# Kernel optimization log

Measured on AMD Instinct MI355X. Metric: run time of the kernel, lower is better.

The kernel has to match this reference:

```python
import jax, jax.numpy as jnp
import numpy as np
from jax import lax

D_MODEL, D_INNER, D_CONV, DT_RANK, D_STATE, SEQ_LEN = 1024, 2048, 4, 64, 16, 4096


def setup_inputs() -> dict:
    key = jax.random.key(0)
    ks = jax.random.split(key, 9)
    s = 0.02
    x = jax.random.normal(ks[0], (SEQ_LEN, D_MODEL), dtype=jnp.float32)
    W_in = jax.random.normal(ks[1], (2 * D_INNER, D_MODEL), dtype=jnp.float32) * s
    conv_w = jax.random.normal(ks[2], (D_INNER, 1, D_CONV), dtype=jnp.float32) * 0.2  # depthwise (O,I/g,K)
    conv_b = jax.random.normal(ks[3], (D_INNER,), dtype=jnp.float32) * s
    W_x = jax.random.normal(ks[4], (DT_RANK + 2 * D_STATE, D_INNER), dtype=jnp.float32) * s
    W_dt = jax.random.normal(ks[5], (D_INNER, DT_RANK), dtype=jnp.float32) * s
    b_dt = jax.random.normal(ks[6], (D_INNER,), dtype=jnp.float32) * s
    # canonical S4D-real init: A[d, n] = n+1 -> A_log = log(1..d_state), tiled over d_inner
    A_log = jnp.log(jnp.tile(jnp.arange(1, D_STATE + 1, dtype=jnp.float32), (D_INNER, 1)))
    D = jnp.ones((D_INNER,), dtype=jnp.float32)
    W_out = jax.random.normal(ks[7], (D_MODEL, D_INNER), dtype=jnp.float32) * s
    return {"x": x, "W_in": W_in, "conv_w": conv_w, "conv_b": conv_b,
            "W_x": W_x, "W_dt": W_dt, "b_dt": b_dt, "A_log": A_log, "D": D,
            "W_out": W_out}


def _causal_depthwise_conv(x_ld, conv_w, conv_b):
    # x_ld: (L, d_inner). eqx Conv1d with padding=d_conv-1 then [:, :L] == left-pad causal conv.
    k = conv_w.shape[-1]
    xp = jnp.pad(x_ld, ((k - 1, 0), (0, 0)))  # (L+k-1, d)
    lhs = xp.T[None]  # (1, d, L+k-1)
    out = lax.conv_general_dilated(
        lhs, conv_w, window_strides=(1,), padding='VALID',
        dimension_numbers=('NCH', 'OIH', 'NCH'),
        feature_group_count=x_ld.shape[1])  # (1, d, L)
    return (out[0] + conv_b[:, None]).T  # (L, d)


def reference(x, W_in, conv_w, conv_b, W_x, W_dt, b_dt, A_log, D, W_out):
    L = x.shape[0]
    d_inner, d_state = A_log.shape
    dt_rank = W_dt.shape[1]

    xr = x @ W_in.T                      # (L, 2*d_inner)
    xi, res = jnp.split(xr, 2, axis=-1)  # each (L, d_inner)
    xs = jax.nn.silu(_causal_depthwise_conv(xi, conv_w, conv_b))  # (L, d_inner)

    # selective SSM
    dbl = xs @ W_x.T                     # (L, dt_rank + 2*d_state)
    dt_in, B, C = jnp.split(dbl, [dt_rank, dt_rank + d_state], axis=-1)
    delta = jax.nn.softplus(dt_in @ W_dt.T + b_dt)       # (L, d_inner)
    A = -jnp.exp(A_log)                                  # (d_inner, d_state)
    dA = jnp.exp(delta[:, :, None] * A[None])            # (L, d, n)
    dBu = delta[:, :, None] * B[:, None, :] * xs[:, :, None]  # (L, d, n)

    def step(h, ab):
        a, b = ab
        h = a * h + b
        return h, h

    _, hs = lax.scan(step, jnp.zeros((d_inner, d_state), dtype=x.dtype), (dA, dBu))
    y = jnp.einsum('ldn,ln->ld', hs, C) + xs * D         # (L, d_inner)

    y = y * jax.nn.silu(res)
    return y @ W_out.T                                   # (L, d_model)
```

## Files before the change

kernel.cpp:

```cpp
#include <hip/hip_runtime.h>
#include <cstdint>
#include <cstddef>

#define LSEQ 4096
#define DM 1024
#define DI 2048
#define DCONV 4
#define DRNK 64
#define DSTATE 16
#define DXW 96
#define NCH 64
#define CLEN 64
#define KSPLIT 8

typedef unsigned short ushort_t;
typedef __bf16 bfx8 __attribute__((ext_vector_type(8)));
typedef float  fx4  __attribute__((ext_vector_type(4)));
typedef ushort_t usx8 __attribute__((ext_vector_type(8)));

__device__ __forceinline__ float siluf(float x) { return x / (1.f + __expf(-x)); }
__device__ __forceinline__ float softplusf(float x) {
  return fmaxf(x, 0.f) + log1pf(__expf(-fabsf(x)));
}
__device__ __forceinline__ ushort_t f2b(float x) {
  __bf16 b = (__bf16)x;
  return __builtin_bit_cast(ushort_t, b);
}
__device__ __forceinline__ float b2f(ushort_t u) {
  unsigned int x = ((unsigned int)u) << 16;
  return __builtin_bit_cast(float, x);
}
__device__ __forceinline__ void async16(const void* g, void* l) {
  __builtin_amdgcn_global_load_lds(
      (const __attribute__((address_space(1))) unsigned int*)g,
      (__attribute__((address_space(3))) unsigned int*)l, 16, 0, 0);
}

template <int EPI, int BN>
__global__ __launch_bounds__(256) void gemm_bf16(
    const ushort_t* __restrict__ A, int lda,
    const ushort_t* __restrict__ B, int ldb,
    void* __restrict__ Cv, int ldc, int K,
    const float* __restrict__ bias)
{
  constexpr int NJ = BN / 32;
  __shared__ ushort_t As[128 * 32];
  __shared__ ushort_t Bs[BN * 32];
  const int tid  = threadIdx.x;
  const int m0   = blockIdx.y * 128, n0 = blockIdx.x * BN;
  const int lane = tid & 63;
  const int wave = tid >> 6;
  const int wm   = (wave >> 1) * 64, wn = (wave & 1) * (BN / 2);
  const int lm   = lane & 15;
  const int r0 = tid >> 2;
  const int cswz = (((tid & 3) ^ ((r0 >> 1) & 3))) * 8;
  const int swz = (((lane >> 4) ^ ((lm >> 1) & 3))) * 8;

  fx4 acc[4][NJ] = {};

  const ushort_t* ga = A + (size_t)(m0 + r0) * lda + cswz;
  const ushort_t* gb = B + (size_t)(n0 + r0) * ldb + cswz;
  ushort_t* la0 = &As[r0 * 32 + (tid & 3) * 8];
  ushort_t* la1 = &As[(r0 + 64) * 32 + (tid & 3) * 8];
  ushort_t* lb0 = &Bs[r0 * 32 + (tid & 3) * 8];
  ushort_t* lb1 = (BN == 128) ? &Bs[(r0 + 64) * 32 + (tid & 3) * 8] : nullptr;

  for (int k0 = 0; k0 < K; k0 += 32) {
    async16(ga + k0, la0);
    async16(ga + (size_t)64 * lda + k0, la1);
    async16(gb + k0, lb0);
    if (BN == 128) async16(gb + (size_t)64 * ldb + k0, lb1);
    __syncthreads();

    bfx8 af[4], bfr[NJ];
#pragma unroll
    for (int i = 0; i < 4; ++i)
      af[i] = *(const bfx8*)&As[(wm + i * 16 + lm) * 32 + swz];
#pragma unroll
    for (int j = 0; j < NJ; ++j)
      bfr[j] = *(const bfx8*)&Bs[(wn + j * 16 + lm) * 32 + swz];
#pragma unroll
    for (int i = 0; i < 4; ++i)
#pragma unroll
      for (int j = 0; j < NJ; ++j)
        acc[i][j] = __builtin_amdgcn_mfma_f32_16x16x32_bf16(af[i], bfr[j], acc[i][j], 0, 0, 0);
    __syncthreads();
  }

  const int crow = (lane >> 4) * 4;
  const int ccol = lane & 15;
#pragma unroll
  for (int i = 0; i < 4; ++i)
#pragma unroll
    for (int r = 0; r < 4; ++r) {
      const size_t rowoff = (size_t)(m0 + wm + i * 16 + crow + r) * ldc + n0 + wn + ccol;
      if (EPI == 1) {
        ushort_t* cp = (ushort_t*)Cv + rowoff;
#pragma unroll
        for (int j = 0; j < NJ; ++j) cp[j * 16] = f2b(acc[i][j][r]);
      } else if (EPI == 2) {
        ushort_t* cp = (ushort_t*)Cv + rowoff;
        const int nb = n0 + wn + ccol;
#pragma unroll
        for (int j = 0; j < NJ; ++j)
          cp[j * 16] = f2b(softplusf(acc[i][j][r] + bias[nb + j * 16]));
      } else {
        float* cp = (float*)Cv + rowoff;
#pragma unroll
        for (int j = 0; j < NJ; ++j) cp[j * 16] = acc[i][j][r];
      }
    }
}

__global__ __launch_bounds__(256) void gemm_dbl(
    const ushort_t* __restrict__ A, const ushort_t* __restrict__ B,
    float* __restrict__ P)
{
  __shared__ ushort_t As[128 * 32];
  __shared__ ushort_t Bs[128 * 32];
  const int tid  = threadIdx.x;
  const int m0   = blockIdx.y * 128;
  const int lane = tid & 63;
  const int wave = tid >> 6;
  const int wm   = (wave >> 1) * 64, wn = (wave & 1) * 48;
  const int lm   = lane & 15;
  const int r0 = tid >> 2;
  const int cswz = (((tid & 3) ^ ((r0 >> 1) & 3))) * 8;
  const int swz  = (((lane >> 4) ^ ((lm >> 1) & 3))) * 8;
  const int kbeg = blockIdx.z * (DI / KSPLIT);

  fx4 acc[4][3] = {};

  const int brow1 = (r0 + 64 < DXW) ? r0 + 64 : DXW - 1;
  const ushort_t* ga  = A + (size_t)(m0 + r0) * DI + kbeg + cswz;
  const ushort_t* gb0 = B + (size_t)r0 * DI + kbeg + cswz;
  const ushort_t* gb1 = B + (size_t)brow1 * DI + kbeg + cswz;
  ushort_t* la0 = &As[r0 * 32 + (tid & 3) * 8];
  ushort_t* la1 = &As[(r0 + 64) * 32 + (tid & 3) * 8];
  ushort_t* lb0 = &Bs[r0 * 32 + (tid & 3) * 8];
  ushort_t* lb1 = &Bs[(r0 + 64) * 32 + (tid & 3) * 8];

  for (int k0 = 0; k0 < DI / KSPLIT; k0 += 32) {
    async16(ga + k0, la0);
    async16(ga + (size_t)64 * DI + k0, la1);
    async16(gb0 + k0, lb0);
    async16(gb1 + k0, lb1);
    __syncthreads();

    bfx8 af[4], bfr[3];
#pragma unroll
    for (int i = 0; i < 4; ++i)
      af[i] = *(const bfx8*)&As[(wm + i * 16 + lm) * 32 + swz];
#pragma unroll
    for (int j = 0; j < 3; ++j)
      bfr[j] = *(const bfx8*)&Bs[(wn + j * 16 + lm) * 32 + swz];
#pragma unroll
    for (int i = 0; i < 4; ++i)
#pragma unroll
      for (int j = 0; j < 3; ++j)
        acc[i][j] = __builtin_amdgcn_mfma_f32_16x16x32_bf16(af[i], bfr[j], acc[i][j], 0, 0, 0);
    __syncthreads();
  }

  float* base = P + (size_t)blockIdx.z * LSEQ * DXW;
  const int crow = (lane >> 4) * 4;
  const int ccol = lane & 15;
#pragma unroll
  for (int i = 0; i < 4; ++i)
#pragma unroll
    for (int r = 0; r < 4; ++r) {
      float* cp = base + (size_t)(m0 + wm + i * 16 + crow + r) * DXW + wn + ccol;
#pragma unroll
      for (int j = 0; j < 3; ++j)
        cp[j * 16] = acc[i][j][r];
    }
}

__global__ __launch_bounds__(256) void reduce_dbl(
    const float* __restrict__ P, ushort_t* __restrict__ dtb,
    float* __restrict__ dblBC)
{
  const int f = blockIdx.x * 256 + threadIdx.x;
  float s = 0.f;
#pragma unroll
  for (int z = 0; z < KSPLIT; ++z) s += P[(size_t)z * LSEQ * DXW + f];
  const int l = f / DXW;
  const int c = f - l * DXW;
  if (c < DRNK) dtb[(size_t)l * DRNK + c] = f2b(s);
  else          dblBC[(size_t)l * 32 + (c - DRNK)] = s;
}

#define CSZ0 (LSEQ * DM)
#define CSZ1 (2 * DI * DM)
#define CSZ2 (DM * DI)
#define CSZ3 (DXW * DI)
#define CSZ4 (DI * DRNK)
#define CTOT (CSZ0 + CSZ1 + CSZ2 + CSZ3 + CSZ4)

__global__ __launch_bounds__(256) void cast_all(
    const float* __restrict__ x, const float* __restrict__ W_in,
    const float* __restrict__ W_out, const float* __restrict__ W_x,
    const float* __restrict__ W_dt,
    ushort_t* __restrict__ xb, ushort_t* __restrict__ W_inb,
    ushort_t* __restrict__ W_outb, ushort_t* __restrict__ W_xb,
    ushort_t* __restrict__ W_dtb)
{
  int i = (blockIdx.x * 256 + threadIdx.x) * 4;
  if (i >= CTOT) return;
  const float* src; ushort_t* dst;
  if (i < CSZ0) { src = x + i; dst = xb + i; }
  else if (i < CSZ0 + CSZ1) { int o = i - CSZ0; src = W_in + o; dst = W_inb + o; }
  else if (i < CSZ0 + CSZ1 + CSZ2) { int o = i - CSZ0 - CSZ1; src = W_out + o; dst = W_outb + o; }
  else if (i < CSZ0 + CSZ1 + CSZ2 + CSZ3) { int o = i - CSZ0 - CSZ1 - CSZ2; src = W_x + o; dst = W_xb + o; }
  else { int o = i - CSZ0 - CSZ1 - CSZ2 - CSZ3; src = W_dt + o; dst = W_dtb + o; }
  float4 v = *(const float4*)src;
  ushort4 o4;
  o4.x = f2b(v.x); o4.y = f2b(v.y); o4.z = f2b(v.z); o4.w = f2b(v.w);
  *(ushort4*)dst = o4;
}

__global__ __launch_bounds__(256) void conv2(
    const ushort_t* __restrict__ xrb, const float* __restrict__ cw,
    const float* __restrict__ cb, ushort_t* __restrict__ xsb)
{
  const int d0 = threadIdx.x * 8;
  const int l0 = blockIdx.x * 8;

  float4 w[8];
#pragma unroll
  for (int j = 0; j < 8; ++j) w[j] = *(const float4*)(cw + (size_t)(d0 + j) * DCONV);
  float cbv[8];
  *(float4*)&cbv[0] = *(const float4*)(cb + d0);
  *(float4*)&cbv[4] = *(const float4*)(cb + d0 + 4);

  float h0[8], h1[8], h2[8];
#pragma unroll
  for (int j = 0; j < 8; ++j) { h0[j] = 0.f; h1[j] = 0.f; h2[j] = 0.f; }
  if (l0 >= 3) {
    usx8 u0 = *(const usx8*)(xrb + (size_t)(l0 - 3) * (2 * DI) + d0);
    usx8 u1 = *(const usx8*)(xrb + (size_t)(l0 - 2) * (2 * DI) + d0);
    usx8 u2 = *(const usx8*)(xrb + (size_t)(l0 - 1) * (2 * DI) + d0);
#pragma unroll
    for (int j = 0; j < 8; ++j) { h0[j] = b2f(u0[j]); h1[j] = b2f(u1[j]); h2[j] = b2f(u2[j]); }
  }

#pragma unroll
  for (int i = 0; i < 8; ++i) {
    const int l = l0 + i;
    usx8 uc = *(const usx8*)(xrb + (size_t)l * (2 * DI) + d0);
    float c[8];
#pragma unroll
    for (int j = 0; j < 8; ++j) c[j] = b2f(uc[j]);
    usx8 o;
#pragma unroll
    for (int j = 0; j < 8; ++j) {
      float acc = cbv[j];
      acc = fmaf(w[j].x, h0[j], acc);
      acc = fmaf(w[j].y, h1[j], acc);
      acc = fmaf(w[j].z, h2[j], acc);
      acc = fmaf(w[j].w, c[j], acc);
      o[j] = f2b(siluf(acc));
    }
    *(usx8*)(xsb + (size_t)l * DI + d0) = o;
#pragma unroll
    for (int j = 0; j < 8; ++j) { h0[j] = h1[j]; h1[j] = h2[j]; h2[j] = c[j]; }
  }
}

__device__ __forceinline__ bool chain_ok(const float* Av) {
  bool ok = true;
#pragma unroll
  for (int n = 0; n < DSTATE; ++n)
    ok = ok && (fabsf(Av[n] + (float)(n + 1)) < 1e-4f);
  return ok;
}

__global__ __launch_bounds__(256) void scan_pass1(
    const ushort_t* __restrict__ deltab, const ushort_t* __restrict__ xsb,
    const float* __restrict__ dblBC, const float* __restrict__ A_log,
    float* __restrict__ cP, float* __restrict__ cS)
{
  const int tid = threadIdx.x;
  const int g = blockIdx.x;
  const int c = blockIdx.y;
  const int d = g * 256 + tid;
  __shared__ ushort_t Dsh[CLEN * 256];
  __shared__ ushort_t Ush[CLEN * 256];
  __shared__ float Bsh[CLEN][DSTATE];

  const size_t rowbase = (size_t)(c * CLEN) * DI + g * 256;
  for (int i = tid; i < CLEN * 32; i += 256) {
    const int l = i >> 5;
    const int o = (i & 31) * 8;
    *(usx8*)&Dsh[l * 256 + o] = *(const usx8*)(deltab + rowbase + (size_t)l * DI + o);
    *(usx8*)&Ush[l * 256 + o] = *(const usx8*)(xsb   + rowbase + (size_t)l * DI + o);
  }
  for (int i = tid; i < CLEN * DSTATE; i += 256) {
    const int l = i >> 4, n = i & 15;
    Bsh[l][n] = dblBC[(size_t)(c * CLEN + l) * 32 + n];
  }
  __syncthreads();

  float Av[DSTATE], h[DSTATE];
#pragma unroll
  for (int n = 0; n < DSTATE; ++n) {
    Av[n] = -__expf(A_log[d * DSTATE + n]);
    h[n] = 0.f;
  }
  const size_t base = (size_t)c * DI * DSTATE + (size_t)d * DSTATE;

  if (chain_ok(Av)) {
    float sd = 0.f;
    for (int l = 0; l < CLEN; ++l) {
      const float dlt = b2f(Dsh[l * 256 + tid]);
      const float du = dlt * b2f(Ush[l * 256 + tid]);
      sd += dlt;
      const float q = __expf(-dlt);
      float dAn = 1.f;
#pragma unroll
      for (int n = 0; n < DSTATE; ++n) {
        dAn *= q;
        h[n] = fmaf(dAn, h[n], du * Bsh[l][n]);
      }
    }
    const float Qc = __expf(-sd);
    float Pn = 1.f;
#pragma unroll
    for (int n = 0; n < DSTATE; ++n) {
      Pn *= Qc;
      cP[base + n] = Pn; cS[base + n] = h[n];
    }
  } else {
    float P[DSTATE];
#pragma unroll
    for (int n = 0; n < DSTATE; ++n) P[n] = 1.f;
    for (int l = 0; l < CLEN; ++l) {
      const float dlt = b2f(Dsh[l * 256 + tid]);
      const float du = dlt * b2f(Ush[l * 256 + tid]);
#pragma unroll
      for (int n = 0; n < DSTATE; ++n) {
        const float dA = __expf(dlt * Av[n]);
        h[n] = fmaf(dA, h[n], du * Bsh[l][n]);
        P[n] *= dA;
      }
    }
#pragma unroll
    for (int n = 0; n < DSTATE; ++n) { cP[base + n] = P[n]; cS[base + n] = h[n]; }
  }
}

__global__ __launch_bounds__(256) void scan_pass2(
    const float* __restrict__ cP, const float* __restrict__ cS,
    float* __restrict__ ch0)
{
  const int dn = blockIdx.x * 256 + threadIdx.x;
  float h = 0.f;
  for (int c = 0; c < NCH; ++c) {
    const size_t o = (size_t)c * DI * DSTATE + dn;
    const float p = cP[o], s = cS[o];
    ch0[o] = h;
    h = fmaf(p, h, s);
  }
}

__global__ __launch_bounds__(256) void scan_pass3(
    const ushort_t* __restrict__ deltab, const ushort_t* __restrict__ xsb,
    const float* __restrict__ dblBC, const float* __restrict__ A_log,
    const float* __restrict__ ch0, const float* __restrict__ Dp,
    const ushort_t* __restrict__ xrb, ushort_t* __restrict__ y1b)
{
  const int tid = threadIdx.x;
  const int g = blockIdx.x;
  const int c = blockIdx.y;
  const int d = g * 256 + tid;
  __shared__ ushort_t Dsh[CLEN * 256];
  __shared__ ushort_t Ush[CLEN * 256];
  __shared__ float Bsh[CLEN][DSTATE];
  __shared__ float Csh[CLEN][DSTATE];

  const size_t rowbase = (size_t)(c * CLEN) * DI + g * 256;
  for (int i = tid; i < CLEN * 32; i += 256) {
    const int l = i >> 5;
    const int o = (i & 31) * 8;
    *(usx8*)&Dsh[l * 256 + o] = *(const usx8*)(deltab + rowbase + (size_t)l * DI + o);
    *(usx8*)&Ush[l * 256 + o] = *(const usx8*)(xsb   + rowbase + (size_t)l * DI + o);
  }
  for (int i = tid; i < CLEN * DSTATE; i += 256) {
    const int l = i >> 4, n = i & 15;
    const size_t row = (size_t)(c * CLEN + l) * 32;
    Bsh[l][n] = dblBC[row + n];
    Csh[l][n] = dblBC[row + 16 + n];
  }
  __syncthreads();

  float Av[DSTATE], h[DSTATE];
  const size_t base = (size_t)c * DI * DSTATE + (size_t)d * DSTATE;
#pragma unroll
  for (int n = 0; n < DSTATE; ++n) {
    Av[n] = -__expf(A_log[d * DSTATE + n]);
    h[n] = ch0[base + n];
  }
  const float Dd = Dp[d];
  const ushort_t* resp = xrb + (size_t)(c * CLEN) * (2 * DI) + DI + d;
  ushort_t* yp = y1b + (size_t)(c * CLEN) * DI + d;

  if (chain_ok(Av)) {
    for (int l = 0; l < CLEN; ++l) {
      const float dlt = b2f(Dsh[l * 256 + tid]);
      const float u = b2f(Ush[l * 256 + tid]);
      const float du = dlt * u;
      const float q = __expf(-dlt);
      float dAn = 1.f;
      float y = 0.f;
#pragma unroll
      for (int n = 0; n < DSTATE; ++n) {
        dAn *= q;
        h[n] = fmaf(dAn, h[n], du * Bsh[l][n]);
        y = fmaf(h[n], Csh[l][n], y);
      }
      y = fmaf(u, Dd, y);
      const float res = b2f(resp[(size_t)l * (2 * DI)]);
      yp[(size_t)l * DI] = f2b(y * siluf(res));
    }
  } else {
    for (int l = 0; l < CLEN; ++l) {
      const float dlt = b2f(Dsh[l * 256 + tid]);
      const float u = b2f(Ush[l * 256 + tid]);
      const float du = dlt * u;
      float y = 0.f;
#pragma unroll
      for (int n = 0; n < DSTATE; ++n) {
        const float dA = __expf(dlt * Av[n]);
        h[n] = fmaf(dA, h[n], du * Bsh[l][n]);
        y = fmaf(h[n], Csh[l][n], y);
      }
      y = fmaf(u, Dd, y);
      const float res = b2f(resp[(size_t)l * (2 * DI)]);
      yp[(size_t)l * DI] = f2b(y * siluf(res));
    }
  }
}

extern "C" void kernel_launch(void* const* d_in, const int* in_sizes, int n_in,
                              void* d_out, int out_size, void* d_ws, size_t ws_size,
                              hipStream_t stream) {
  (void)in_sizes; (void)n_in; (void)out_size; (void)ws_size;
  const float* x      = (const float*)d_in[0];
  const float* W_in   = (const float*)d_in[1];
  const float* conv_w = (const float*)d_in[2];
  const float* conv_b = (const float*)d_in[3];
  const float* W_x    = (const float*)d_in[4];
  const float* W_dt   = (const float*)d_in[5];
  const float* b_dt   = (const float*)d_in[6];
  const float* A_log  = (const float*)d_in[7];
  const float* Dp     = (const float*)d_in[8];
  const float* W_out  = (const float*)d_in[9];
  float* out = (float*)d_out;

  float* ws    = (float*)d_ws;
  float* cP    = ws;
  float* cS    = cP + (size_t)NCH * DI * DSTATE;
  ushort_t* deltab = (ushort_t*)(cS + (size_t)NCH * DI * DSTATE);
  ushort_t* xrb   = deltab + (size_t)LSEQ * DI;
  ushort_t* xsb   = xrb   + (size_t)LSEQ * 2 * DI;
  ushort_t* y1b   = xsb   + (size_t)LSEQ * DI;
  ushort_t* xb    = y1b   + (size_t)LSEQ * DI;
  ushort_t* W_inb = xb    + (size_t)LSEQ * DM;
  ushort_t* W_outb= W_inb + (size_t)2 * DI * DM;
  ushort_t* W_xb  = W_outb+ (size_t)DM * DI;
  ushort_t* W_dtb = W_xb  + (size_t)DXW * DI;
  ushort_t* dtb   = W_dtb + (size_t)DI * DRNK;
  float* dblBC = (float*)(dtb + (size_t)LSEQ * DRNK);
  float* partial = cP;
  float* ch0 = cP;

  hipLaunchKernelGGL(cast_all, dim3((CTOT / 4 + 255) / 256), dim3(256), 0, stream,
                     x, W_in, W_out, W_x, W_dt, xb, W_inb, W_outb, W_xb, W_dtb);

  hipLaunchKernelGGL(HIP_KERNEL_NAME(gemm_bf16<1, 128>),
                     dim3((2 * DI) / 128, LSEQ / 128), dim3(256), 0, stream,
                     xb, DM, W_inb, DM, (void*)xrb, 2 * DI, DM, nullptr);

  hipLaunchKernelGGL(conv2, dim3(LSEQ / 8), dim3(256), 0, stream,
                     xrb, conv_w, conv_b, xsb);

  hipLaunchKernelGGL(gemm_dbl, dim3(1, LSEQ / 128, KSPLIT), dim3(256), 0, stream,
                     xsb, W_xb, partial);
  hipLaunchKernelGGL(reduce_dbl, dim3((LSEQ * DXW) / 256), dim3(256), 0, stream,
                     partial, dtb, dblBC);

  hipLaunchKernelGGL(HIP_KERNEL_NAME(gemm_bf16<2, 128>),
                     dim3(DI / 128, LSEQ / 128), dim3(256), 0, stream,
                     dtb, DRNK, W_dtb, DRNK, (void*)deltab, DI, DRNK, b_dt);

  hipLaunchKernelGGL(scan_pass1, dim3(DI / 256, NCH), dim3(256), 0, stream,
                     deltab, xsb, dblBC, A_log, cP, cS);
  hipLaunchKernelGGL(scan_pass2, dim3((DI * DSTATE) / 256), dim3(256), 0, stream,
                     cP, cS, ch0);
  hipLaunchKernelGGL(scan_pass3, dim3(DI / 256, NCH), dim3(256), 0, stream,
                     deltab, xsb, dblBC, A_log, ch0, Dp, xrb, y1b);

  hipLaunchKernelGGL(HIP_KERNEL_NAME(gemm_bf16<0, 64>),
                     dim3(DM / 64, LSEQ / 128), dim3(256), 0, stream,
                     y1b, DI, W_outb, DI, (void*)out, DM, DI, nullptr);
}
```

Before: 309.0 us.

## Fuse three-pass chunked scan into one kernel with inter-block atomic flags

Merges the per-chunk scan, the cross-chunk prefix pass and the output scan into a single kernel. Blocks publish chunk summaries and signal through per-group atomic counters; a subset of blocks runs the cross-chunk prefix and signals completion while the others wait. The delta and xs tiles are loaded into shared memory once instead of twice, and two kernel launches are removed. In exchange it relies on all 512 blocks being resident at the same time for the spin-waits to make progress, adds busy-waiting, and bounds the spin loops with a timeout that could silently let blocks proceed with incomplete data.

```diff
diff --git a/kernel.cpp b/kernel.cpp
--- a/kernel.cpp
+++ b/kernel.cpp
@@ -203,8 +203,9 @@
     const float* __restrict__ W_dt,
     ushort_t* __restrict__ xb, ushort_t* __restrict__ W_inb,
     ushort_t* __restrict__ W_outb, ushort_t* __restrict__ W_xb,
-    ushort_t* __restrict__ W_dtb)
+    ushort_t* __restrict__ W_dtb, int* __restrict__ flags)
 {
+  if (blockIdx.x == 0 && threadIdx.x < 16) flags[threadIdx.x] = 0;
   int i = (blockIdx.x * 256 + threadIdx.x) * 4;
   if (i >= CTOT) return;
   const float* src; ushort_t* dst;
@@ -275,100 +276,16 @@
   return ok;
 }
 
-__global__ __launch_bounds__(256) void scan_pass1(
+__global__ __launch_bounds__(256) void scan_fused(
     const ushort_t* __restrict__ deltab, const ushort_t* __restrict__ xsb,
     const float* __restrict__ dblBC, const float* __restrict__ A_log,
-    float* __restrict__ cP, float* __restrict__ cS)
+    const float* __restrict__ Dp, const ushort_t* __restrict__ xrb,
+    ushort_t* __restrict__ y1b,
+    float* __restrict__ cP, float* __restrict__ cS, float* __restrict__ ch0,
+    int* __restrict__ flags)
 {
-  const int tid = threadIdx.x;
-  const int g = blockIdx.x;
-  const int c = blockIdx.y;
-  const int d = g * 256 + tid;
-  __shared__ ushort_t Dsh[CLEN * 256];
-  __shared__ ushort_t Ush[CLEN * 256];
-  __shared__ float Bsh[CLEN][DSTATE];
-
-  const size_t rowbase = (size_t)(c * CLEN) * DI + g * 256;
-  for (int i = tid; i < CLEN * 32; i += 256) {
-    const int l = i >> 5;
-    const int o = (i & 31) * 8;
-    *(usx8*)&Dsh[l * 256 + o] = *(const usx8*)(deltab + rowbase + (size_t)l * DI + o);
-    *(usx8*)&Ush[l * 256 + o] = *(const usx8*)(xsb   + rowbase + (size_t)l * DI + o);
-  }
-  for (int i = tid; i < CLEN * DSTATE; i += 256) {
-    const int l = i >> 4, n = i & 15;
-    Bsh[l][n] = dblBC[(size_t)(c * CLEN + l) * 32 + n];
-  }
-  __syncthreads();
-
-  float Av[DSTATE], h[DSTATE];
-#pragma unroll
-  for (int n = 0; n < DSTATE; ++n) {
-    Av[n] = -__expf(A_log[d * DSTATE + n]);
-    h[n] = 0.f;
-  }
-  const size_t base = (size_t)c * DI * DSTATE + (size_t)d * DSTATE;
-
-  if (chain_ok(Av)) {
-    float sd = 0.f;
-    for (int l = 0; l < CLEN; ++l) {
-      const float dlt = b2f(Dsh[l * 256 + tid]);
-      const float du = dlt * b2f(Ush[l * 256 + tid]);
-      sd += dlt;
-      const float q = __expf(-dlt);
-      float dAn = 1.f;
-#pragma unroll
-      for (int n = 0; n < DSTATE; ++n) {
-        dAn *= q;
-        h[n] = fmaf(dAn, h[n], du * Bsh[l][n]);
-      }
-    }
-    const float Qc = __expf(-sd);
-    float Pn = 1.f;
-#pragma unroll
-    for (int n = 0; n < DSTATE; ++n) {
-      Pn *= Qc;
-      cP[base + n] = Pn; cS[base + n] = h[n];
-    }
-  } else {
-    float P[DSTATE];
-#pragma unroll
-    for (int n = 0; n < DSTATE; ++n) P[n] = 1.f;
-    for (int l = 0; l < CLEN; ++l) {
-      const float dlt = b2f(Dsh[l * 256 + tid]);
-      const float du = dlt * b2f(Ush[l * 256 + tid]);
-#pragma unroll
-      for (int n = 0; n < DSTATE; ++n) {
-        const float dA = __expf(dlt * Av[n]);
-        h[n] = fmaf(dA, h[n], du * Bsh[l][n]);
-        P[n] *= dA;
-      }
-    }
-#pragma unroll
-    for (int n = 0; n < DSTATE; ++n) { cP[base + n] = P[n]; cS[base + n] = h[n]; }
-  }
-}
-
-__global__ __launch_bounds__(256) void scan_pass2(
-    const float* __restrict__ cP, const float* __restrict__ cS,
-    float* __restrict__ ch0)
-{
-  const int dn = blockIdx.x * 256 + threadIdx.x;
-  float h = 0.f;
-  for (int c = 0; c < NCH; ++c) {
-    const size_t o = (size_t)c * DI * DSTATE + dn;
-    const float p = cP[o], s = cS[o];
-    ch0[o] = h;
-    h = fmaf(p, h, s);
-  }
-}
-
-__global__ __launch_bounds__(256) void scan_pass3(
-    const ushort_t* __restrict__ deltab, const ushort_t* __restrict__ xsb,
-    const float* __restrict__ dblBC, const float* __restrict__ A_log,
-    const float* __restrict__ ch0, const float* __restrict__ Dp,
-    const ushort_t* __restrict__ xrb, ushort_t* __restrict__ y1b)
-{
+  int* cntP = flags;
+  int* cntC = flags + 8;
   const int tid = threadIdx.x;
   const int g = blockIdx.x;
   const int c = blockIdx.y;
@@ -394,17 +311,97 @@
   __syncthreads();
 
   float Av[DSTATE], h[DSTATE];
-  const size_t base = (size_t)c * DI * DSTATE + (size_t)d * DSTATE;
 #pragma unroll
   for (int n = 0; n < DSTATE; ++n) {
     Av[n] = -__expf(A_log[d * DSTATE + n]);
-    h[n] = ch0[base + n];
-  }
+    h[n] = 0.f;
+  }
+  const bool chain = chain_ok(Av);
+  const size_t base = (size_t)c * DI * DSTATE + (size_t)d * DSTATE;
+
+  if (chain) {
+    float sd = 0.f;
+    for (int l = 0; l < CLEN; ++l) {
+      const float dlt = b2f(Dsh[l * 256 + tid]);
+      const float du = dlt * b2f(Ush[l * 256 + tid]);
+      sd += dlt;
+      const float q = __expf(-dlt);
+      float dAn = 1.f;
+#pragma unroll
+      for (int n = 0; n < DSTATE; ++n) {
+        dAn *= q;
+        h[n] = fmaf(dAn, h[n], du * Bsh[l][n]);
+      }
+    }
+    const float Qc = __expf(-sd);
+    float Pn = 1.f;
+#pragma unroll
+    for (int n = 0; n < DSTATE; ++n) {
+      Pn *= Qc;
+      cP[base + n] = Pn; cS[base + n] = h[n];
+    }
+  } else {
+    float P[DSTATE];
+#pragma unroll
+    for (int n = 0; n < DSTATE; ++n) P[n] = 1.f;
+    for (int l = 0; l < CLEN; ++l) {
+      const float dlt = b2f(Dsh[l * 256 + tid]);
+      const float du = dlt * b2f(Ush[l * 256 + tid]);
+#pragma unroll
+      for (int n = 0; n < DSTATE; ++n) {
+        const float dA = __expf(dlt * Av[n]);
+        h[n] = fmaf(dA, h[n], du * Bsh[l][n]);
+        P[n] *= dA;
+      }
+    }
+#pragma unroll
+    for (int n = 0; n < DSTATE; ++n) { cP[base + n] = P[n]; cS[base + n] = h[n]; }
+  }
+
+  __syncthreads();
+  if (tid == 0)
+    __hip_atomic_fetch_add(&cntP[g], 1, __ATOMIC_RELEASE, __HIP_MEMORY_SCOPE_AGENT);
+
+  const int bid = c * 8 + g;
+  if (bid < (DI * DSTATE) / 256) {
+    const int gs = bid >> 4;
+    if (tid == 0) {
+      long spin = 0;
+      while (__hip_atomic_load(&cntP[gs], __ATOMIC_ACQUIRE, __HIP_MEMORY_SCOPE_AGENT) < NCH) {
+        __builtin_amdgcn_s_sleep(8);
+        if (++spin > (1L << 22)) break;
+      }
+    }
+    __syncthreads();
+    const int dn = bid * 256 + tid;
+    float hh = 0.f;
+    for (int cc = 0; cc < NCH; ++cc) {
+      const size_t o = (size_t)cc * DI * DSTATE + dn;
+      const float p = cP[o], s = cS[o];
+      ch0[o] = hh;
+      hh = fmaf(p, hh, s);
+    }
+    __syncthreads();
+    if (tid == 0)
+      __hip_atomic_fetch_add(&cntC[gs], 1, __ATOMIC_RELEASE, __HIP_MEMORY_SCOPE_AGENT);
+  }
+
+  if (tid == 0) {
+    long spin = 0;
+    while (__hip_atomic_load(&cntC[g], __ATOMIC_ACQUIRE, __HIP_MEMORY_SCOPE_AGENT) < 16) {
+      __builtin_amdgcn_s_sleep(8);
+      if (++spin > (1L << 22)) break;
+    }
+  }
+  __syncthreads();
+
+#pragma unroll
+  for (int n = 0; n < DSTATE; ++n) h[n] = ch0[base + n];
   const float Dd = Dp[d];
   const ushort_t* resp = xrb + (size_t)(c * CLEN) * (2 * DI) + DI + d;
   ushort_t* yp = y1b + (size_t)(c * CLEN) * DI + d;
 
-  if (chain_ok(Av)) {
+  if (chain) {
     for (int l = 0; l < CLEN; ++l) {
       const float dlt = b2f(Dsh[l * 256 + tid]);
       const float u = b2f(Ush[l * 256 + tid]);
@@ -471,11 +468,13 @@
   ushort_t* W_dtb = W_xb  + (size_t)DXW * DI;
   ushort_t* dtb   = W_dtb + (size_t)DI * DRNK;
   float* dblBC = (float*)(dtb + (size_t)LSEQ * DRNK);
+  int* flags = (int*)(dblBC + (size_t)LSEQ * 32);
   float* partial = cP;
   float* ch0 = cP;
 
   hipLaunchKernelGGL(cast_all, dim3((CTOT / 4 + 255) / 256), dim3(256), 0, stream,
-                     x, W_in, W_out, W_x, W_dt, xb, W_inb, W_outb, W_xb, W_dtb);
+                     x, W_in, W_out, W_x, W_dt, xb, W_inb, W_outb, W_xb, W_dtb,
+                     flags);
 
   hipLaunchKernelGGL(HIP_KERNEL_NAME(gemm_bf16<1, 128>),
                      dim3((2 * DI) / 128, LSEQ / 128), dim3(256), 0, stream,
@@ -493,12 +492,9 @@
                      dim3(DI / 128, LSEQ / 128), dim3(256), 0, stream,
                      dtb, DRNK, W_dtb, DRNK, (void*)deltab, DI, DRNK, b_dt);
 
-  hipLaunchKernelGGL(scan_pass1, dim3(DI / 256, NCH), dim3(256), 0, stream,
-                     deltab, xsb, dblBC, A_log, cP, cS);
-  hipLaunchKernelGGL(scan_pass2, dim3((DI * DSTATE) / 256), dim3(256), 0, stream,
-                     cP, cS, ch0);
-  hipLaunchKernelGGL(scan_pass3, dim3(DI / 256, NCH), dim3(256), 0, stream,
-                     deltab, xsb, dblBC, A_log, ch0, Dp, xrb, y1b);
+  hipLaunchKernelGGL(scan_fused, dim3(DI / 256, NCH), dim3(256), 0, stream,
+                     deltab, xsb, dblBC, A_log, Dp, xrb, y1b, cP, cS, ch0,
+                     flags);
 
   hipLaunchKernelGGL(HIP_KERNEL_NAME(gemm_bf16<0, 64>),
                      dim3(DM / 64, LSEQ / 128), dim3(256), 0, stream,
```

New measurement: 417.5 us. 1.35x slower.
